# Optimization experiments

Hardware: AMD Instinct MI355X
Metric: run time of the kernel (lower is better)

## Reference

```python
import jax, jax.numpy as jnp
import numpy as np

H = 2048       # hidden_size
NH = 16        # num_attention_heads
HN = H // NH   # per-head dim = 128
B = 2
S = 2048
ALPHA = 32.0   # cogview pb-relax alpha


def setup_inputs() -> dict:
    key = jax.random.key(0)
    k1, k2, k3 = jax.random.split(key, 3)
    hidden_states = jax.random.normal(k1, (B, S, H), dtype=jnp.float32)
    # causal lower-triangular float mask [1,1,s,s]
    ltor_mask = jnp.tril(jnp.ones((S, S), dtype=jnp.float32))[None, None]
    # fused QKV projection params (torch Linear: y = x @ W.T + b)
    lim_qkv = 1.0 / np.sqrt(H)
    W_qkv = jax.random.uniform(k2, (3 * H, H), jnp.float32, -lim_qkv, lim_qkv)
    b_qkv = jnp.zeros((3 * H,), jnp.float32)
    W_out = jax.random.uniform(k3, (H, H), jnp.float32, -lim_qkv, lim_qkv)
    b_out = jnp.zeros((H,), jnp.float32)
    return {"hidden_states": hidden_states, "ltor_mask": ltor_mask,
            "W_qkv": W_qkv, "b_qkv": b_qkv, "W_out": W_out, "b_out": b_out}


def reference(hidden_states, ltor_mask, W_qkv, b_qkv, W_out, b_out):
    b, s, h = hidden_states.shape
    # fused QKV projection: [b,s,3h]
    qkv = hidden_states @ W_qkv.T + b_qkv
    q, k, v = jnp.split(qkv, 3, axis=-1)
    # [b,s,h] -> [b,n,s,hn]
    def heads(t):
        return t.reshape(b, s, NH, HN).transpose(0, 2, 1, 3)
    q, k, v = heads(q), heads(k), heads(v)
    # cogview_pb_relax: scale query before matmul
    scores = jnp.einsum('bnqd,bnkd->bnqk', q / jnp.sqrt(jnp.float32(HN)), k)
    mask = ltor_mask[:, :, -scores.shape[-2]:]
    scores = scores * mask - 10000.0 * (1.0 - mask)
    # pb-relax max rescaling (max is detached)
    scaled = scores / ALPHA
    maxes = jax.lax.stop_gradient(jnp.max(scaled.reshape(b, NH, -1), axis=-1))
    scores = (scaled - maxes[:, :, None, None]) * ALPHA
    probs = jax.nn.softmax(scores, axis=-1)
    ctx = jnp.einsum('bnqk,bnkd->bnqd', probs, v)
    ctx = ctx.transpose(0, 2, 1, 3).reshape(b, s, h)
    out = ctx @ W_out.T + b_out
    return out
```

## Files before the change

### kernel.cpp

```cpp
#include <hip/hip_runtime.h>

typedef __bf16 bf16;
typedef bf16 bf16x4 __attribute__((ext_vector_type(4)));
typedef bf16 bf16x8 __attribute__((ext_vector_type(8)));
typedef float f32x4 __attribute__((ext_vector_type(4)));

#define Bb 2
#define Ss 2048
#define Hh 2048
#define NHh 16
#define HNd 128
#define H3 6144
#define Mm 4096
#define SCALE_QK 0.08838834764831843f

__device__ __forceinline__ void async_copy16(void* lds, const void* g) {
  __builtin_amdgcn_global_load_lds(
      (const __attribute__((address_space(1))) unsigned int*)g,
      (__attribute__((address_space(3))) unsigned int*)lds, 16, 0, 0);
}

__global__ __launch_bounds__(256) void cvt_kernel(const float* __restrict__ in,
                                                  bf16* __restrict__ out, int n) {
  int i = (blockIdx.x * 256 + threadIdx.x) * 4;
  if (i < n) {
    float4 v = *reinterpret_cast<const float4*>(in + i);
    bf16x4 o;
    o[0] = (bf16)v.x; o[1] = (bf16)v.y; o[2] = (bf16)v.z; o[3] = (bf16)v.w;
    *reinterpret_cast<bf16x4*>(out + i) = o;
  }
}


struct G192Frags {
  bf16x8 af[2][2];
  bf16x8 bfr[3][2];
};

template <int MP, int RDB>
__device__ __forceinline__ void g192_reads(const bf16* asb, const bf16* bsb,
                                           int lm, int lg, int wm, int wn,
                                           G192Frags& f) {
  if (RDB) {
#pragma unroll
    for (int nj = 0; nj < 3; ++nj)
#pragma unroll
      for (int kk = 0; kk < 2; ++kk) {
        const int row = wn * 48 + nj * 16 + lm;
        f.bfr[nj][kk] = *reinterpret_cast<const bf16x8*>(
            (const char*)bsb + row * 128 + ((kk * 64 + lg * 16) ^ ((lm & 7) << 4)));
      }
  }
#pragma unroll
  for (int i = 0; i < 2; ++i)
#pragma unroll
    for (int kk = 0; kk < 2; ++kk) {
      const int row = wm * 128 + (MP * 2 + i) * 16 + lm;
      f.af[i][kk] = *reinterpret_cast<const bf16x8*>(
          (const char*)asb + row * 128 + ((kk * 64 + lg * 16) ^ ((lm & 7) << 4)));
    }
}

template <int MP>
__device__ __forceinline__ void g192_mfma(const G192Frags& f, f32x4 (&acc)[8][3]) {
#pragma unroll
  for (int kk = 0; kk < 2; ++kk)
#pragma unroll
    for (int i = 0; i < 2; ++i)
#pragma unroll
      for (int nj = 0; nj < 3; ++nj)
        acc[MP * 2 + i][nj] = __builtin_amdgcn_mfma_f32_16x16x32_bf16(
            f.af[i][kk], f.bfr[nj][kk], acc[MP * 2 + i][nj], 0, 0, 0);
}

template <int OUT_F32>
__global__ __launch_bounds__(512, 2) void gemm192_kernel(
    const bf16* __restrict__ A, const bf16* __restrict__ Bw,
    const float* __restrict__ bias, void* __restrict__ Cout,
    int M, int N, int K) {
  __shared__ __align__(16) bf16 As[2][256 * 64];
  __shared__ __align__(16) bf16 Bs[2][192 * 64];

  const int tid = threadIdx.x;
  const int lane = tid & 63;
  const int w = tid >> 6;
  const int wm = w >> 2, wn = w & 3;
  const int lm = lane & 15, lg = lane >> 4;
  const int srow = lane >> 3;
  const int sslot = lane & 7;

  const int id = blockIdx.y * gridDim.x + blockIdx.x;
  const int xcd = id & 7, rem = id >> 3;
  const int bx = xcd * 4 + (rem & 3);
  const int by = rem >> 2;
  const int m0 = by * 256, n0 = bx * 192;

  auto stageA = [&](int b, int t) {
#pragma unroll
    for (int l = 0; l < 4; ++l) {
      const int r = l * 64 + w * 8 + srow;
      async_copy16((char*)&As[b][0] + l * 8192 + w * 1024,
                   A + (size_t)(m0 + r) * K + t * 64 + (sslot ^ srow) * 8);
    }
  };
  auto stageB = [&](int b, int t) {
#pragma unroll
    for (int l = 0; l < 3; ++l) {
      const int r = l * 64 + w * 8 + srow;
      async_copy16((char*)&Bs[b][0] + l * 8192 + w * 1024,
                   Bw + (size_t)(n0 + r) * K + t * 64 + (sslot ^ srow) * 8);
    }
  };

  f32x4 acc[8][3] = {};
  G192Frags f;

#define PHASE(BS, MP, RDB, VM, ...)                                            \
  do {                                                                         \
    g192_reads<MP, RDB>(&As[BS][0], &Bs[BS][0], lm, lg, wm, wn, f);            \
    __VA_ARGS__;                                                               \
    __builtin_amdgcn_s_barrier();                                              \
    __builtin_amdgcn_s_setprio(1);                                             \
    g192_mfma<MP>(f, acc);                                                     \
    __builtin_amdgcn_s_setprio(0);                                             \
    if ((VM) == 3) asm volatile("s_waitcnt vmcnt(3)" ::: "memory");            \
    else if ((VM) == 0) asm volatile("s_waitcnt vmcnt(0)" ::: "memory");       \
    __builtin_amdgcn_s_barrier();                                              \
  } while (0)

  const int nt = K >> 6;
  stageB(0, 0);
  stageA(0, 0);
  stageB(1, 1);
  asm volatile("s_waitcnt vmcnt(3)" ::: "memory");
  __builtin_amdgcn_s_barrier();

#pragma unroll 1
  for (int t = 0; t < nt - 2; t += 2) {
    PHASE(0, 0, 1, 9, stageA(1, t + 1));
    PHASE(0, 1, 0, 9, stageB(0, t + 2));
    PHASE(0, 2, 0, 9, );
    PHASE(0, 3, 0, 3, );
    PHASE(1, 0, 1, 9, stageA(0, t + 2));
    PHASE(1, 1, 0, 9, stageB(1, t + 3));
    PHASE(1, 2, 0, 9, );
    PHASE(1, 3, 0, 3, );
  }
  PHASE(0, 0, 1, 9, stageA(1, nt - 1));
  PHASE(0, 1, 0, 9, );
  PHASE(0, 2, 0, 9, );
  PHASE(0, 3, 0, 0, );
  PHASE(1, 0, 1, 9, );
  PHASE(1, 1, 0, 9, );
  PHASE(1, 2, 0, 9, );
  PHASE(1, 3, 0, 9, );
#undef PHASE

#pragma unroll
  for (int mi = 0; mi < 8; ++mi) {
#pragma unroll
    for (int nj = 0; nj < 3; ++nj) {
      const int col = n0 + wn * 48 + nj * 16 + lm;
      const float bv = bias[col];
      const int r0 = m0 + wm * 128 + mi * 16 + lg * 4;
#pragma unroll
      for (int r = 0; r < 4; ++r) {
        const float v = acc[mi][nj][r] + bv;
        if (OUT_F32)
          reinterpret_cast<float*>(Cout)[(size_t)(r0 + r) * N + col] = v;
        else
          reinterpret_cast<bf16*>(Cout)[(size_t)(r0 + r) * N + col] = (bf16)v;
      }
    }
  }
}

template <int OUT_F32>
__global__ __launch_bounds__(256) void gemm_bt_kernel(
    const bf16* __restrict__ A, const bf16* __restrict__ Bw,
    const float* __restrict__ bias, void* __restrict__ Cout,
    int M, int N, int K) {
  __shared__ __align__(16) bf16 As[128][64];
  __shared__ __align__(16) bf16 Bs[128][64];

  const int tid = threadIdx.x;
  const int lane = tid & 63;
  const int w = tid >> 6;
  const int wr = w >> 1, wc = w & 1;
  const int m0 = blockIdx.y * 128;
  const int n0 = blockIdx.x * 128;
  const int srow = lane >> 3;
  const int sslot = lane & 7;

  f32x4 acc[4][4] = {};

  for (int k0 = 0; k0 < K; k0 += 64) {
#pragma unroll
    for (int c = 0; c < 4; ++c) {
      const int ci = c * 4 + w;
      const int row = ci * 8 + srow;
      async_copy16((char*)&As[0][0] + ci * 1024,
                   A + (size_t)(m0 + row) * K + k0 + sslot * 8);
      async_copy16((char*)&Bs[0][0] + ci * 1024,
                   Bw + (size_t)(n0 + row) * K + k0 + sslot * 8);
    }
    __syncthreads();

#pragma unroll
    for (int kk = 0; kk < 2; ++kk) {
      const int kc = kk * 32 + (lane >> 4) * 8;
      bf16x8 af[4], bfr[4];
#pragma unroll
      for (int mi = 0; mi < 4; ++mi)
        af[mi] = *reinterpret_cast<const bf16x8*>(&As[wr * 64 + mi * 16 + (lane & 15)][kc]);
#pragma unroll
      for (int nj = 0; nj < 4; ++nj)
        bfr[nj] = *reinterpret_cast<const bf16x8*>(&Bs[wc * 64 + nj * 16 + (lane & 15)][kc]);
#pragma unroll
      for (int mi = 0; mi < 4; ++mi)
#pragma unroll
        for (int nj = 0; nj < 4; ++nj)
          acc[mi][nj] = __builtin_amdgcn_mfma_f32_16x16x32_bf16(af[mi], bfr[nj], acc[mi][nj], 0, 0, 0);
    }
    __syncthreads();
  }

#pragma unroll
  for (int mi = 0; mi < 4; ++mi) {
#pragma unroll
    for (int nj = 0; nj < 4; ++nj) {
      const int col = n0 + wc * 64 + nj * 16 + (lane & 15);
      const float bv = bias[col];
      const int r0 = m0 + wr * 64 + mi * 16 + (lane >> 4) * 4;
#pragma unroll
      for (int r = 0; r < 4; ++r) {
        const float v = acc[mi][nj][r] + bv;
        if (OUT_F32)
          reinterpret_cast<float*>(Cout)[(size_t)(r0 + r) * N + col] = v;
        else
          reinterpret_cast<bf16*>(Cout)[(size_t)(r0 + r) * N + col] = (bf16)v;
      }
    }
  }
}

__device__ __forceinline__ void attn_tile(
    const char* ksb, const char* vtb, bf16* psw,
    const bf16x8* qf, f32x4* acc, float* mrow, float* lrow,
    int qr0, int kv0, bool diag, int lm, int lg) {
  float p[4][4];
#pragma unroll
  for (int kt = 0; kt < 4; ++kt) {
    f32x4 s = {};
    const int r = kt * 16 + lm;
#pragma unroll
    for (int kk = 0; kk < 4; ++kk) {
      bf16x8 kf = *reinterpret_cast<const bf16x8*>(
          ksb + r * 256 + ((kk * 64 + lg * 16) ^ ((lm & 7) << 4)));
      s = __builtin_amdgcn_mfma_f32_16x16x32_bf16(qf[kk], kf, s, 0, 0, 0);
    }
    if (diag) {
      const int col = kv0 + kt * 16 + lm;
#pragma unroll
      for (int rr = 0; rr < 4; ++rr)
        p[kt][rr] = (col <= qr0 + lg * 4 + rr) ? s[rr] * SCALE_QK : -3.0e38f;
    } else {
#pragma unroll
      for (int rr = 0; rr < 4; ++rr) p[kt][rr] = s[rr] * SCALE_QK;
    }
  }
#pragma unroll
  for (int rr = 0; rr < 4; ++rr) {
    float pm = fmaxf(fmaxf(p[0][rr], p[1][rr]), fmaxf(p[2][rr], p[3][rr]));
#pragma unroll
    for (int off = 1; off < 16; off <<= 1) pm = fmaxf(pm, __shfl_xor(pm, off));
    const float mnew = fmaxf(mrow[rr], pm);
    const float sc = __expf(mrow[rr] - mnew);
    mrow[rr] = mnew;
    float sum = 0.f;
#pragma unroll
    for (int kt = 0; kt < 4; ++kt) { p[kt][rr] = __expf(p[kt][rr] - mnew); sum += p[kt][rr]; }
#pragma unroll
    for (int off = 1; off < 16; off <<= 1) sum += __shfl_xor(sum, off);
    lrow[rr] = lrow[rr] * sc + sum;
#pragma unroll
    for (int dt = 0; dt < 8; ++dt) acc[dt][rr] *= sc;
  }
#pragma unroll
  for (int kt = 0; kt < 4; ++kt)
#pragma unroll
    for (int rr = 0; rr < 4; ++rr)
      psw[(lg * 4 + rr) * 72 + kt * 16 + lm] = (bf16)p[kt][rr];
  __syncthreads();
#pragma unroll
  for (int kb = 0; kb < 2; ++kb) {
    bf16x8 pa = *reinterpret_cast<const bf16x8*>(&psw[lm * 72 + kb * 32 + lg * 8]);
#pragma unroll
    for (int dt = 0; dt < 8; ++dt) {
      const int d = dt * 16 + lm;
      bf16x8 vf = *reinterpret_cast<const bf16x8*>(
          vtb + d * 128 + ((kb * 64 + lg * 16) ^ (((dt * 2 + (lm >> 3)) & 7) << 4)));
      acc[dt] = __builtin_amdgcn_mfma_f32_16x16x32_bf16(pa, vf, acc[dt], 0, 0, 0);
    }
  }
}

__global__ __launch_bounds__(256, 2) void attn_kernel(const bf16* __restrict__ qkv,
                                                      bf16* __restrict__ ctx) {
  __shared__ __align__(16) bf16 Ks[64 * 128];
  __shared__ __align__(16) bf16 Vt[128 * 64];
  __shared__ __align__(16) bf16 Ps[4 * 16 * 72];

  const int tid = threadIdx.x;
  const int lane = tid & 63;
  const int w = tid >> 6;
  const int lm = lane & 15;
  const int lg = lane >> 4;
  const int pr = blockIdx.x;
  const int bh = blockIdx.y;
  const int b = bh >> 4;
  const int h = bh & 15;
  const int qtA = 31 - pr;
  const int qtB = pr;

  const size_t rs = H3;
  const bf16* qbase = qkv + (size_t)b * Ss * rs + (size_t)h * HNd;
  const bf16* kbase = qbase + Hh;
  const bf16* vbase = qbase + 2 * Hh;

  const int qrA = qtA * 64 + w * 16;
  const int qrB = qtB * 64 + w * 16;

  bf16x8 qfA[4], qfB[4];
#pragma unroll
  for (int kk = 0; kk < 4; ++kk) {
    qfA[kk] = *reinterpret_cast<const bf16x8*>(qbase + (size_t)(qrA + lm) * rs + kk * 32 + lg * 8);
    qfB[kk] = *reinterpret_cast<const bf16x8*>(qbase + (size_t)(qrB + lm) * rs + kk * 32 + lg * 8);
  }

  f32x4 accA[8] = {}, accB[8] = {};
  float mA[4], lA[4], mB[4], lB[4];
#pragma unroll
  for (int r = 0; r < 4; ++r) { mA[r] = mB[r] = -3.0e38f; lA[r] = lB[r] = 0.f; }

  char* ksb = (char*)Ks;
  char* vtb = (char*)Vt;
  bf16* psw = Ps + w * 16 * 72;

  const int nkv = qtA + 1;
  for (int t = 0; t < nkv; ++t) {
    const int kv0 = t * 64;
#pragma unroll
    for (int c = 0; c < 4; ++c) {
      const int ci = c * 4 + w;
      const int row = ci * 4 + lg;
      async_copy16(ksb + ci * 1024,
                   kbase + (size_t)(kv0 + row) * rs + (lm ^ (row & 7)) * 8);
    }
#pragma unroll
    for (int j = 0; j < 4; ++j) {
      const int idx = j * 256 + tid;
      const int kv = idx >> 4;
      const int d8 = idx & 15;
      bf16x8 v = *reinterpret_cast<const bf16x8*>(vbase + (size_t)(kv0 + kv) * rs + d8 * 8);
#pragma unroll
      for (int e = 0; e < 8; ++e)
        *reinterpret_cast<bf16*>(vtb + (d8 * 8 + e) * 128 + ((kv * 2) ^ ((d8 & 7) << 4))) = v[e];
    }
    __syncthreads();

    attn_tile(ksb, vtb, psw, qfA, accA, mA, lA, qrA, kv0, t == qtA, lm, lg);
    if (t <= qtB)
      attn_tile(ksb, vtb, psw, qfB, accB, mB, lB, qrB, kv0, t == qtB, lm, lg);
    __syncthreads();
  }

  bf16* cbase = ctx + (size_t)b * Ss * Hh + (size_t)h * HNd;
#pragma unroll
  for (int dt = 0; dt < 8; ++dt)
#pragma unroll
    for (int r = 0; r < 4; ++r) {
      cbase[(size_t)(qrA + lg * 4 + r) * Hh + dt * 16 + lm] = (bf16)(accA[dt][r] / lA[r]);
      cbase[(size_t)(qrB + lg * 4 + r) * Hh + dt * 16 + lm] = (bf16)(accB[dt][r] / lB[r]);
    }
}

extern "C" void kernel_launch(void* const* d_in, const int* in_sizes, int n_in,
                              void* d_out, int out_size, void* d_ws, size_t ws_size,
                              hipStream_t stream) {
  const float* hidden = (const float*)d_in[0];
  const float* Wqkv = (const float*)d_in[2];
  const float* bqkv = (const float*)d_in[3];
  const float* Wout = (const float*)d_in[4];
  const float* bout = (const float*)d_in[5];
  float* out = (float*)d_out;

  char* ws = (char*)d_ws;
  bf16* hid_bf = (bf16*)ws;  ws += (size_t)Mm * Hh * 2;
  bf16* wqkv_bf = (bf16*)ws; ws += (size_t)H3 * Hh * 2;
  bf16* wout_bf = (bf16*)ws; ws += (size_t)Hh * Hh * 2;
  bf16* qkv_bf = (bf16*)ws;  ws += (size_t)Mm * H3 * 2;
  bf16* ctx_bf = (bf16*)ws;  ws += (size_t)Mm * Hh * 2;

  cvt_kernel<<<(Mm * Hh / 4 + 255) / 256, 256, 0, stream>>>(hidden, hid_bf, Mm * Hh);
  cvt_kernel<<<(H3 * Hh / 4 + 255) / 256, 256, 0, stream>>>(Wqkv, wqkv_bf, H3 * Hh);
  cvt_kernel<<<(Hh * Hh / 4 + 255) / 256, 256, 0, stream>>>(Wout, wout_bf, Hh * Hh);

  gemm192_kernel<0><<<dim3(H3 / 192, Mm / 256), 512, 0, stream>>>(
      hid_bf, wqkv_bf, bqkv, qkv_bf, Mm, H3, Hh);
  attn_kernel<<<dim3(16, Bb * NHh), 256, 0, stream>>>(qkv_bf, ctx_bf);
  gemm_bt_kernel<1><<<dim3(Hh / 128, Mm / 128), 256, 0, stream>>>(
      ctx_bf, wout_bf, bout, out, Mm, Hh, Hh);
}
```

Measured before the change: 299.4 us.

## Double-buffer K/V tiles in attention, reuse pipelined GEMM for output projection

The attention kernel now double-buffers the K and V tiles. The next tile's K is fetched asynchronously and its V is held in registers while the current tile computes, and the V transpose is written as packed 32-bit pairs. The 192-wide pipelined GEMM is generalized over N-tile width, and the output projection switches from the simple 128x128 kernel to the 256x128 variant with 512 threads. This targets global-load latency in attention and the weaker output GEMM, at the cost of more LDS and register pressure in attention.

```diff
diff --git a/kernel.cpp b/kernel.cpp
--- a/kernel.cpp
+++ b/kernel.cpp
@@ -3,6 +3,7 @@
 typedef __bf16 bf16;
 typedef bf16 bf16x4 __attribute__((ext_vector_type(4)));
 typedef bf16 bf16x8 __attribute__((ext_vector_type(8)));
+typedef unsigned short u16x8 __attribute__((ext_vector_type(8)));
 typedef float f32x4 __attribute__((ext_vector_type(4)));
 
 #define Bb 2
@@ -20,6 +21,13 @@
       (__attribute__((address_space(3))) unsigned int*)lds, 16, 0, 0);
 }
 
+template <int N>
+__device__ __forceinline__ void waitvm() {
+  if constexpr (N == 0) asm volatile("s_waitcnt vmcnt(0)" ::: "memory");
+  else if constexpr (N == 2) asm volatile("s_waitcnt vmcnt(2)" ::: "memory");
+  else if constexpr (N == 3) asm volatile("s_waitcnt vmcnt(3)" ::: "memory");
+}
+
 __global__ __launch_bounds__(256) void cvt_kernel(const float* __restrict__ in,
                                                   bf16* __restrict__ out, int n) {
   int i = (blockIdx.x * 256 + threadIdx.x) * 4;
@@ -31,22 +39,22 @@
   }
 }
 
-
-struct G192Frags {
+template <int NJ>
+struct GFrags {
   bf16x8 af[2][2];
-  bf16x8 bfr[3][2];
+  bf16x8 bfr[NJ][2];
 };
 
-template <int MP, int RDB>
-__device__ __forceinline__ void g192_reads(const bf16* asb, const bf16* bsb,
-                                           int lm, int lg, int wm, int wn,
-                                           G192Frags& f) {
+template <int NJ, int MP, int RDB>
+__device__ __forceinline__ void g_reads(const bf16* asb, const bf16* bsb,
+                                        int lm, int lg, int wm, int wn,
+                                        GFrags<NJ>& f) {
   if (RDB) {
 #pragma unroll
-    for (int nj = 0; nj < 3; ++nj)
+    for (int nj = 0; nj < NJ; ++nj)
 #pragma unroll
       for (int kk = 0; kk < 2; ++kk) {
-        const int row = wn * 48 + nj * 16 + lm;
+        const int row = wn * (NJ * 16) + nj * 16 + lm;
         f.bfr[nj][kk] = *reinterpret_cast<const bf16x8*>(
             (const char*)bsb + row * 128 + ((kk * 64 + lg * 16) ^ ((lm & 7) << 4)));
       }
@@ -61,25 +69,25 @@
     }
 }
 
-template <int MP>
-__device__ __forceinline__ void g192_mfma(const G192Frags& f, f32x4 (&acc)[8][3]) {
+template <int NJ, int MP>
+__device__ __forceinline__ void g_mfma(const GFrags<NJ>& f, f32x4 (&acc)[8][NJ]) {
 #pragma unroll
   for (int kk = 0; kk < 2; ++kk)
 #pragma unroll
     for (int i = 0; i < 2; ++i)
 #pragma unroll
-      for (int nj = 0; nj < 3; ++nj)
+      for (int nj = 0; nj < NJ; ++nj)
         acc[MP * 2 + i][nj] = __builtin_amdgcn_mfma_f32_16x16x32_bf16(
             f.af[i][kk], f.bfr[nj][kk], acc[MP * 2 + i][nj], 0, 0, 0);
 }
 
-template <int OUT_F32>
-__global__ __launch_bounds__(512, 2) void gemm192_kernel(
+template <int NJ, int OUT_F32>
+__global__ __launch_bounds__(512, 2) void gemmW_kernel(
     const bf16* __restrict__ A, const bf16* __restrict__ Bw,
     const float* __restrict__ bias, void* __restrict__ Cout,
     int M, int N, int K) {
   __shared__ __align__(16) bf16 As[2][256 * 64];
-  __shared__ __align__(16) bf16 Bs[2][192 * 64];
+  __shared__ __align__(16) bf16 Bs[2][NJ * 64 * 64];
 
   const int tid = threadIdx.x;
   const int lane = tid & 63;
@@ -90,10 +98,11 @@
   const int sslot = lane & 7;
 
   const int id = blockIdx.y * gridDim.x + blockIdx.x;
+  const int cpx = gridDim.x >> 3;
   const int xcd = id & 7, rem = id >> 3;
-  const int bx = xcd * 4 + (rem & 3);
-  const int by = rem >> 2;
-  const int m0 = by * 256, n0 = bx * 192;
+  const int bx = xcd * cpx + rem % cpx;
+  const int by = rem / cpx;
+  const int m0 = by * 256, n0 = bx * (NJ * 64);
 
   auto stageA = [&](int b, int t) {
 #pragma unroll
@@ -105,26 +114,25 @@
   };
   auto stageB = [&](int b, int t) {
 #pragma unroll
-    for (int l = 0; l < 3; ++l) {
+    for (int l = 0; l < NJ; ++l) {
       const int r = l * 64 + w * 8 + srow;
       async_copy16((char*)&Bs[b][0] + l * 8192 + w * 1024,
                    Bw + (size_t)(n0 + r) * K + t * 64 + (sslot ^ srow) * 8);
     }
   };
 
-  f32x4 acc[8][3] = {};
-  G192Frags f;
+  f32x4 acc[8][NJ] = {};
+  GFrags<NJ> f;
 
 #define PHASE(BS, MP, RDB, VM, ...)                                            \
   do {                                                                         \
-    g192_reads<MP, RDB>(&As[BS][0], &Bs[BS][0], lm, lg, wm, wn, f);            \
+    g_reads<NJ, MP, RDB>(&As[BS][0], &Bs[BS][0], lm, lg, wm, wn, f);           \
     __VA_ARGS__;                                                               \
     __builtin_amdgcn_s_barrier();                                              \
     __builtin_amdgcn_s_setprio(1);                                             \
-    g192_mfma<MP>(f, acc);                                                     \
+    g_mfma<NJ, MP>(f, acc);                                                    \
     __builtin_amdgcn_s_setprio(0);                                             \
-    if ((VM) == 3) asm volatile("s_waitcnt vmcnt(3)" ::: "memory");            \
-    else if ((VM) == 0) asm volatile("s_waitcnt vmcnt(0)" ::: "memory");       \
+    waitvm<(VM)>();                                                            \
     __builtin_amdgcn_s_barrier();                                              \
   } while (0)
 
@@ -132,7 +140,7 @@
   stageB(0, 0);
   stageA(0, 0);
   stageB(1, 1);
-  asm volatile("s_waitcnt vmcnt(3)" ::: "memory");
+  waitvm<NJ>();
   __builtin_amdgcn_s_barrier();
 
 #pragma unroll 1
@@ -140,11 +148,11 @@
     PHASE(0, 0, 1, 9, stageA(1, t + 1));
     PHASE(0, 1, 0, 9, stageB(0, t + 2));
     PHASE(0, 2, 0, 9, );
-    PHASE(0, 3, 0, 3, );
+    PHASE(0, 3, 0, NJ, );
     PHASE(1, 0, 1, 9, stageA(0, t + 2));
     PHASE(1, 1, 0, 9, stageB(1, t + 3));
     PHASE(1, 2, 0, 9, );
-    PHASE(1, 3, 0, 3, );
+    PHASE(1, 3, 0, NJ, );
   }
   PHASE(0, 0, 1, 9, stageA(1, nt - 1));
   PHASE(0, 1, 0, 9, );
@@ -159,8 +167,8 @@
 #pragma unroll
   for (int mi = 0; mi < 8; ++mi) {
 #pragma unroll
-    for (int nj = 0; nj < 3; ++nj) {
-      const int col = n0 + wn * 48 + nj * 16 + lm;
+    for (int nj = 0; nj < NJ; ++nj) {
+      const int col = n0 + wn * (NJ * 16) + nj * 16 + lm;
       const float bv = bias[col];
       const int r0 = m0 + wm * 128 + mi * 16 + lg * 4;
 #pragma unroll
@@ -175,75 +183,6 @@
   }
 }
 
-template <int OUT_F32>
-__global__ __launch_bounds__(256) void gemm_bt_kernel(
-    const bf16* __restrict__ A, const bf16* __restrict__ Bw,
-    const float* __restrict__ bias, void* __restrict__ Cout,
-    int M, int N, int K) {
-  __shared__ __align__(16) bf16 As[128][64];
-  __shared__ __align__(16) bf16 Bs[128][64];
-
-  const int tid = threadIdx.x;
-  const int lane = tid & 63;
-  const int w = tid >> 6;
-  const int wr = w >> 1, wc = w & 1;
-  const int m0 = blockIdx.y * 128;
-  const int n0 = blockIdx.x * 128;
-  const int srow = lane >> 3;
-  const int sslot = lane & 7;
-
-  f32x4 acc[4][4] = {};
-
-  for (int k0 = 0; k0 < K; k0 += 64) {
-#pragma unroll
-    for (int c = 0; c < 4; ++c) {
-      const int ci = c * 4 + w;
-      const int row = ci * 8 + srow;
-      async_copy16((char*)&As[0][0] + ci * 1024,
-                   A + (size_t)(m0 + row) * K + k0 + sslot * 8);
-      async_copy16((char*)&Bs[0][0] + ci * 1024,
-                   Bw + (size_t)(n0 + row) * K + k0 + sslot * 8);
-    }
-    __syncthreads();
-
-#pragma unroll
-    for (int kk = 0; kk < 2; ++kk) {
-      const int kc = kk * 32 + (lane >> 4) * 8;
-      bf16x8 af[4], bfr[4];
-#pragma unroll
-      for (int mi = 0; mi < 4; ++mi)
-        af[mi] = *reinterpret_cast<const bf16x8*>(&As[wr * 64 + mi * 16 + (lane & 15)][kc]);
-#pragma unroll
-      for (int nj = 0; nj < 4; ++nj)
-        bfr[nj] = *reinterpret_cast<const bf16x8*>(&Bs[wc * 64 + nj * 16 + (lane & 15)][kc]);
-#pragma unroll
-      for (int mi = 0; mi < 4; ++mi)
-#pragma unroll
-        for (int nj = 0; nj < 4; ++nj)
-          acc[mi][nj] = __builtin_amdgcn_mfma_f32_16x16x32_bf16(af[mi], bfr[nj], acc[mi][nj], 0, 0, 0);
-    }
-    __syncthreads();
-  }
-
-#pragma unroll
-  for (int mi = 0; mi < 4; ++mi) {
-#pragma unroll
-    for (int nj = 0; nj < 4; ++nj) {
-      const int col = n0 + wc * 64 + nj * 16 + (lane & 15);
-      const float bv = bias[col];
-      const int r0 = m0 + wr * 64 + mi * 16 + (lane >> 4) * 4;
-#pragma unroll
-      for (int r = 0; r < 4; ++r) {
-        const float v = acc[mi][nj][r] + bv;
-        if (OUT_F32)
-          reinterpret_cast<float*>(Cout)[(size_t)(r0 + r) * N + col] = v;
-        else
-          reinterpret_cast<bf16*>(Cout)[(size_t)(r0 + r) * N + col] = (bf16)v;
-      }
-    }
-  }
-}
-
 __device__ __forceinline__ void attn_tile(
     const char* ksb, const char* vtb, bf16* psw,
     const bf16x8* qf, f32x4* acc, float* mrow, float* lrow,
@@ -307,8 +246,8 @@
 
 __global__ __launch_bounds__(256, 2) void attn_kernel(const bf16* __restrict__ qkv,
                                                       bf16* __restrict__ ctx) {
-  __shared__ __align__(16) bf16 Ks[64 * 128];
-  __shared__ __align__(16) bf16 Vt[128 * 64];
+  __shared__ __align__(16) bf16 Ks[2][64 * 128];
+  __shared__ __align__(16) bf16 Vt[2][128 * 64];
   __shared__ __align__(16) bf16 Ps[4 * 16 * 72];
 
   const int tid = threadIdx.x;
@@ -343,13 +282,9 @@
 #pragma unroll
   for (int r = 0; r < 4; ++r) { mA[r] = mB[r] = -3.0e38f; lA[r] = lB[r] = 0.f; }
 
-  char* ksb = (char*)Ks;
-  char* vtb = (char*)Vt;
   bf16* psw = Ps + w * 16 * 72;
 
-  const int nkv = qtA + 1;
-  for (int t = 0; t < nkv; ++t) {
-    const int kv0 = t * 64;
+  auto stageK = [&](char* ksb, int kv0) {
 #pragma unroll
     for (int c = 0; c < 4; ++c) {
       const int ci = c * 4 + w;
@@ -357,21 +292,57 @@
       async_copy16(ksb + ci * 1024,
                    kbase + (size_t)(kv0 + row) * rs + (lm ^ (row & 7)) * 8);
     }
-#pragma unroll
-    for (int j = 0; j < 4; ++j) {
-      const int idx = j * 256 + tid;
-      const int kv = idx >> 4;
+  };
+  auto loadV = [&](int kv0, bf16x8* vr) {
+#pragma unroll
+    for (int jj = 0; jj < 2; ++jj) {
+      const int idx = jj * 256 + tid;
+      const int pair = idx >> 4;
       const int d8 = idx & 15;
-      bf16x8 v = *reinterpret_cast<const bf16x8*>(vbase + (size_t)(kv0 + kv) * rs + d8 * 8);
-#pragma unroll
-      for (int e = 0; e < 8; ++e)
-        *reinterpret_cast<bf16*>(vtb + (d8 * 8 + e) * 128 + ((kv * 2) ^ ((d8 & 7) << 4))) = v[e];
-    }
-    __syncthreads();
-
-    attn_tile(ksb, vtb, psw, qfA, accA, mA, lA, qrA, kv0, t == qtA, lm, lg);
+      vr[jj * 2 + 0] = *reinterpret_cast<const bf16x8*>(
+          vbase + (size_t)(kv0 + pair * 2) * rs + d8 * 8);
+      vr[jj * 2 + 1] = *reinterpret_cast<const bf16x8*>(
+          vbase + (size_t)(kv0 + pair * 2 + 1) * rs + d8 * 8);
+    }
+  };
+  auto writeV = [&](char* vtb, const bf16x8* vr) {
+#pragma unroll
+    for (int jj = 0; jj < 2; ++jj) {
+      const int idx = jj * 256 + tid;
+      const int pair = idx >> 4;
+      const int d8 = idx & 15;
+      const u16x8 lo = (u16x8)vr[jj * 2 + 0];
+      const u16x8 hi = (u16x8)vr[jj * 2 + 1];
+#pragma unroll
+      for (int e = 0; e < 8; ++e) {
+        const unsigned pk = (unsigned)lo[e] | ((unsigned)hi[e] << 16);
+        *reinterpret_cast<unsigned*>(
+            vtb + (d8 * 8 + e) * 128 + ((pair * 4) ^ ((d8 & 7) << 4))) = pk;
+      }
+    }
+  };
+
+  bf16x8 vr[4];
+  stageK((char*)Ks[0], 0);
+  loadV(0, vr);
+  writeV((char*)Vt[0], vr);
+  __syncthreads();
+
+  const int nkv = qtA + 1;
+  for (int t = 0; t < nkv; ++t) {
+    const int cur = t & 1;
+    const bool pf = (t + 1 < nkv);
+    if (pf) {
+      stageK((char*)Ks[cur ^ 1], (t + 1) * 64);
+      loadV((t + 1) * 64, vr);
+    }
+    const int kv0 = t * 64;
+    attn_tile((char*)Ks[cur], (char*)Vt[cur], psw, qfA, accA, mA, lA, qrA, kv0,
+              t == qtA, lm, lg);
     if (t <= qtB)
-      attn_tile(ksb, vtb, psw, qfB, accB, mB, lB, qrB, kv0, t == qtB, lm, lg);
+      attn_tile((char*)Ks[cur], (char*)Vt[cur], psw, qfB, accB, mB, lB, qrB, kv0,
+                t == qtB, lm, lg);
+    if (pf) writeV((char*)Vt[cur ^ 1], vr);
     __syncthreads();
   }
 
@@ -406,9 +377,9 @@
   cvt_kernel<<<(H3 * Hh / 4 + 255) / 256, 256, 0, stream>>>(Wqkv, wqkv_bf, H3 * Hh);
   cvt_kernel<<<(Hh * Hh / 4 + 255) / 256, 256, 0, stream>>>(Wout, wout_bf, Hh * Hh);
 
-  gemm192_kernel<0><<<dim3(H3 / 192, Mm / 256), 512, 0, stream>>>(
+  gemmW_kernel<3, 0><<<dim3(H3 / 192, Mm / 256), 512, 0, stream>>>(
       hid_bf, wqkv_bf, bqkv, qkv_bf, Mm, H3, Hh);
   attn_kernel<<<dim3(16, Bb * NHh), 256, 0, stream>>>(qkv_bf, ctx_bf);
-  gemm_bt_kernel<1><<<dim3(Hh / 128, Mm / 128), 256, 0, stream>>>(
+  gemmW_kernel<2, 1><<<dim3(Hh / 128, Mm / 256), 512, 0, stream>>>(
       ctx_bf, wout_bf, bout, out, Mm, Hh, Hh);
 }
```

After: 276.8 us. 1.08x faster.
